# Performance work log

Measured on AMD Instinct MI355X. Metric: run time of the kernel, lower is better.

Reference implementation:

```python
import jax, jax.numpy as jnp
import numpy as np

B, T, H, V = 32, 256, 1024, 256


def setup_inputs() -> dict:
    key = jax.random.key(0)
    ks = jax.random.split(key, 12)
    xavier = float(np.sqrt(6.0 / (H + V)))
    inp = {
        "x": jax.random.randint(ks[0], (B, T), 0, V, dtype=jnp.int64),
        "targets": jax.random.randint(ks[1], (B, T), 0, V, dtype=jnp.int64),
        "h0": jnp.zeros((B, H), jnp.float32),
        "c0": jnp.zeros((B, H), jnp.float32),
        "h1": jnp.zeros((B, H), jnp.float32),
        "c1": jnp.zeros((B, H), jnp.float32),
        # learned params
        "emb": jax.random.normal(ks[2], (V, H), jnp.float32) * 0.05,
        "W_ih0": jax.random.normal(ks[3], (H, 4 * H), jnp.float32) / np.sqrt(H),
        "W_hh0": jax.random.normal(ks[4], (H, 4 * H), jnp.float32) / np.sqrt(H),
        "b0": jnp.zeros((4 * H,), jnp.float32),
        "W_ih1": jax.random.normal(ks[5], (H, 4 * H), jnp.float32) / np.sqrt(H),
        "W_hh1": jax.random.normal(ks[6], (H, 4 * H), jnp.float32) / np.sqrt(H),
        "b1": jnp.zeros((4 * H,), jnp.float32),
        "W_out": jax.random.uniform(ks[7], (H, V), jnp.float32, -xavier, xavier),
        "b_out": jnp.zeros((V,), jnp.float32),
    }
    return inp


def _lstm_cell(h, c, inp, W_ih, W_hh, b):
    # gates: [B, 4H] -> i, f, g, o
    z = inp @ W_ih + h @ W_hh + b
    i, f, g, o = jnp.split(z, 4, axis=-1)
    c_new = jax.nn.sigmoid(f) * c + jax.nn.sigmoid(i) * jnp.tanh(g)
    h_new = jax.nn.sigmoid(o) * jnp.tanh(c_new)
    return h_new, c_new


def reference(x, targets, h0, c0, h1, c1, emb, W_ih0, W_hh0, b0,
              W_ih1, W_hh1, b1, W_out, b_out):
    # Teacher-forcing branch: embed targets, feed embedding at every step.
    embeddings = emb[targets]            # [B, T, H]
    e_seq = jnp.swapaxes(embeddings, 0, 1)  # [T, B, H] for scan over time

    def step(carry, e_t):
        (h0, c0), (h1, c1) = carry
        h0, c0 = _lstm_cell(h0, c0, e_t, W_ih0, W_hh0, b0)
        h1, c1 = _lstm_cell(h1, c1, h0, W_ih1, W_hh1, b1)
        logit = h1 @ W_out + b_out       # [B, V]
        return ((h0, c0), (h1, c1)), logit

    carry0 = ((h0, c0), (h1, c1))
    carry_f, logits_tbv = jax.lax.scan(step, carry0, e_seq)
    logits = jnp.swapaxes(logits_tbv, 0, 1)  # [B, T, V]
    (h0f, c0f), (h1f, c1f) = carry_f
    return logits, h0f, c0f, h1f, c1f
```

## Files before the change

kernel.cpp:

```cpp
#include <hip/hip_runtime.h>
#include <cstdint>


typedef float    f32x4 __attribute__((ext_vector_type(4)));
typedef short    s16x8 __attribute__((ext_vector_type(8)));
typedef unsigned u32x4 __attribute__((ext_vector_type(4)));

#define DEV __device__ __forceinline__

DEV unsigned short f2bf(float x){
  unsigned u = __builtin_bit_cast(unsigned, x);
  unsigned r = (u + 0x7fffu + ((u >> 16) & 1u)) >> 16;
  return (unsigned short)r;
}
DEV float bf2f(unsigned short b){ return __builtin_bit_cast(float, ((unsigned)b) << 16); }

DEV s16x8 ld16(const void* p){ return *(const s16x8*)p; }

DEV f32x4 MF(s16x8 a, s16x8 b, f32x4 c){
  return __builtin_amdgcn_mfma_f32_16x16x32_bf16(a, b, c, 0, 0, 0);
}

#define LDC(dst, ptr)  asm volatile("global_load_dwordx4 %0, %1, off sc0 sc1" : "=v"(dst) : "v"(ptr))
#define LDP(dst, ptr)  asm volatile("global_load_dwordx4 %0, %1, off"         : "=v"(dst) : "v"(ptr))
#define WAITVM(n) do { asm volatile("s_waitcnt vmcnt(" #n ")" ::: "memory"); \
                       __builtin_amdgcn_sched_barrier(0); } while (0)
#define CFENCE()  asm volatile("" ::: "memory")
#define TRIPLE(Cmn, Ahm, Alm, Bhn, Bln) do { \
    Cmn = MF(Ahm, Bhn, Cmn); Cmn = MF(Ahm, Bln, Cmn); Cmn = MF(Alm, Bhn, Cmn); } while (0)

DEV void st16c(void* p, u32x4 v){
  asm volatile("global_store_dwordx4 %0, %1, off sc0 sc1" :: "v"(p), "v"(v) : "memory");
}
DEV void set_flag(int* p, int v){
  __hip_atomic_store(p, v, __ATOMIC_RELAXED, __HIP_MEMORY_SCOPE_AGENT);
}
template<int SLP>
DEV void pollT(const int* f, int lane, int target){
  const int* p0 = f + lane * 8;
  const int* p1 = f + (64 + lane) * 8;
  for (;;) {
    int a = __hip_atomic_load(p0, __ATOMIC_RELAXED, __HIP_MEMORY_SCOPE_AGENT);
    int b = __hip_atomic_load(p1, __ATOMIC_RELAXED, __HIP_MEMORY_SCOPE_AGENT);
    if (__all((a >= target) && (b >= target))) break;
    __builtin_amdgcn_s_sleep(SLP);
  }
  CFENCE();
}
DEV char* h0slot(char* wa0, char* s0, char* hi, int s){
  return (s == 0) ? s0 : ((s <= 128) ? wa0 + ((size_t)(s - 1) << 17)
                                     : hi  + ((size_t)(s - 129) << 17));
}

DEV void halfgemm8(const char* smemMat, const char* ALb, const char* Bb,
                   int wgl, int ksb, int lane, f32x4 (&C)[2][2]) {
  s16x8 P[3][4], AL[3][2];
  #pragma unroll
  for (int d = 0; d < 2; ++d) {
    #pragma unroll
    for (int q = 0; q < 4; ++q) LDP(P[d][q], Bb + ((q * 32 + ksb + d) << 10) + lane * 16);
    LDP(AL[d][0], ALb + ((((wgl * 2 + 0) * 2 + 1) * 32 + ksb + d) << 10) + lane * 16);
    LDP(AL[d][1], ALb + ((((wgl * 2 + 1) * 2 + 1) * 32 + ksb + d) << 10) + lane * 16);
  }
  #pragma unroll
  for (int i = 0; i < 8; ++i) {
    const int ks = ksb + i;
    if (i < 6) {
      #pragma unroll
      for (int q = 0; q < 4; ++q) LDP(P[(i + 2) % 3][q], Bb + ((q * 32 + ks + 2) << 10) + lane * 16);
      LDP(AL[(i + 2) % 3][0], ALb + ((((wgl * 2 + 0) * 2 + 1) * 32 + ks + 2) << 10) + lane * 16);
      LDP(AL[(i + 2) % 3][1], ALb + ((((wgl * 2 + 1) * 2 + 1) * 32 + ks + 2) << 10) + lane * 16);
    }
    s16x8 Ah0 = ld16(smemMat + ((0 * 32 + ks) << 10) + lane * 16);
    s16x8 Ah1 = ld16(smemMat + ((1 * 32 + ks) << 10) + lane * 16);
    if (i < 6) { WAITVM(12); } else if (i == 6) { WAITVM(6); } else { WAITVM(0); }
    TRIPLE(C[0][0], Ah0, AL[i % 3][0], P[i % 3][0], P[i % 3][2]);
    TRIPLE(C[0][1], Ah0, AL[i % 3][0], P[i % 3][1], P[i % 3][3]);
    TRIPLE(C[1][0], Ah1, AL[i % 3][1], P[i % 3][0], P[i % 3][2]);
    TRIPLE(C[1][1], Ah1, AL[i % 3][1], P[i % 3][1], P[i % 3][3]);
  }
}

__global__ void prep_wfrag(const float* __restrict__ W0, const float* __restrict__ W1,
                           const float* __restrict__ W2, const float* __restrict__ W3,
                           char* D0, char* D1, char* D2, char* D3) {
  int gid = blockIdx.x * 256 + threadIdx.x;
  int lane = gid & 63, ks = (gid >> 6) & 31, jb = (gid >> 11) & 255, mat = gid >> 19;
  const float* S = (mat == 0) ? W0 : (mat == 1) ? W1 : (mat == 2) ? W2 : W3;
  char* D = (mat == 0) ? D0 : (mat == 1) ? D1 : (mat == 2) ? D2 : D3;
  int jp = jb * 16 + (lane & 15), u = jp >> 2, g = jp & 3;
  int kb = ks * 32 + (lane >> 4) * 8;
  s16x8 vh, vl;
  #pragma unroll
  for (int i = 0; i < 8; ++i) {
    float x = S[(kb + i) * 4096 + g * 1024 + u];
    unsigned short h = f2bf(x);
    vh[i] = (short)h;
    vl[i] = (short)f2bf(x - bf2f(h));
  }
  *(s16x8*)(D + (((jb * 2 + 0) * 32 + ks) << 10) + lane * 16) = vh;
  *(s16x8*)(D + (((jb * 2 + 1) * 32 + ks) << 10) + lane * 16) = vl;
}

__global__ void prep_bfrag(const float* __restrict__ emb, const float* __restrict__ Wout,
                           char* Demb, char* Dwout) {
  int gid = blockIdx.x * 256 + threadIdx.x;
  int lane = gid & 63, ks = (gid >> 6) & 31, vb = (gid >> 11) & 15, which = gid >> 15;
  int v = vb * 16 + (lane & 15), kb = ks * 32 + (lane >> 4) * 8;
  s16x8 vh, vl;
  #pragma unroll
  for (int i = 0; i < 8; ++i) {
    float x = which ? Wout[(kb + i) * 256 + v] : emb[v * 1024 + kb + i];
    unsigned short h = f2bf(x);
    vh[i] = (short)h;
    vl[i] = (short)f2bf(x - bf2f(h));
  }
  char* D = which ? Dwout : Demb;
  *(s16x8*)(D + (((vb * 2 + 0) * 32 + ks) << 10) + lane * 16) = vh;
  *(s16x8*)(D + (((vb * 2 + 1) * 32 + ks) << 10) + lane * 16) = vl;
}

__global__ void prep_hinit(const float* __restrict__ h0, const float* __restrict__ h1,
                           char* h0s0, char* h1f) {
  int gid = blockIdx.x * 256 + threadIdx.x;
  int lane = gid & 63, ks = (gid >> 6) & 31, nt = (gid >> 11) & 1, which = gid >> 12;
  const float* S = which ? h1 : h0;
  char* D = which ? h1f : h0s0;
  int b = nt * 16 + (lane & 15), kb = ks * 32 + (lane >> 4) * 8;
  s16x8 vh, vl;
  #pragma unroll
  for (int i = 0; i < 8; ++i) {
    float x = S[b * 1024 + kb + i];
    unsigned short h = f2bf(x);
    vh[i] = (short)h;
    vl[i] = (short)f2bf(x - bf2f(h));
  }
  *(s16x8*)(D + (((0 * 2 + nt) * 32 + ks) << 10) + lane * 16) = vh;
  *(s16x8*)(D + (((1 * 2 + nt) * 32 + ks) << 10) + lane * 16) = vl;
}

__global__ void prep_misc(const float* __restrict__ b1, float* b1i, int* f0a, int* f1a) {
  int i = blockIdx.x * 256 + threadIdx.x;
  if (i < 4096) b1i[i] = b1[(i & 3) * 1024 + (i >> 2)];
  if (i < 1024) { f0a[i] = -1; f1a[i] = -1; }
}

__global__ __launch_bounds__(256, 1) void lstm_persist(
    const int* __restrict__ tgt,
    const float* __restrict__ c0_in, const float* __restrict__ c1_in,
    const float* __restrict__ b0, const float* __restrict__ b_out,
    char* __restrict__ WA0, const char* __restrict__ WA1, const char* __restrict__ WA2,
    const char* __restrict__ WAi0, const char* __restrict__ WoutB, const char* __restrict__ embB,
    float* __restrict__ E0, const float* __restrict__ b1i,
    char* __restrict__ h0s0, char* __restrict__ h0hi, char* __restrict__ h1frag,
    int* __restrict__ f0, int* __restrict__ f1,
    float* __restrict__ out)
{
  extern __shared__ char smem[];
  constexpr int PART = 131072;
  constexpr int RP   = 131072 + 16384;
  const int tid = threadIdx.x, lane = tid & 63, wv = tid >> 6;
  const int wg = blockIdx.x;
  const bool isL0 = (wg < 128);
  const int wgl = isL0 ? wg : (wg - 128);
  const int l15 = lane & 15, l4 = lane >> 4;
  const int mi_e = wv >> 1, nt_e = wv & 1;

  __builtin_amdgcn_fence(__ATOMIC_ACQUIRE, "agent");

  if (isL0) {
    u32x4 tmp[8];
    for (int blk = 0; blk < 4; ++blk) {
      #pragma unroll
      for (int q = 0; q < 8; ++q) {
        int idx = tid + (blk * 8 + q) * 256;
        int l16 = idx & 63, ks = (idx >> 6) & 31, mi = (idx >> 11) & 1, part = idx >> 12;
        LDC(tmp[q], WA0 + ((((wgl * 2 + mi) * 2 + part) * 32 + ks) << 10) + l16 * 16);
      }
      WAITVM(0);
      #pragma unroll
      for (int q = 0; q < 8; ++q) {
        int idx = tid + (blk * 8 + q) * 256;
        int l16 = idx & 63, ks = (idx >> 6) & 31, mi = (idx >> 11) & 1, part = idx >> 12;
        *(u32x4*)(smem + (((part * 2 + mi) * 32 + ks) << 10) + l16 * 16) = tmp[q];
      }
    }
  } else {
    for (int idx = tid; idx < 8192; idx += 256) {
      int l16 = idx & 63, ks = (idx >> 6) & 31, mi = (idx >> 11) & 1, mat = idx >> 12;
      const char* W = mat ? WA2 : WA1;
      u32x4 v = *(const u32x4*)(W + ((((wgl * 2 + mi) * 2 + 0) * 32 + ks) << 10) + l16 * 16);
      *(u32x4*)(smem + (((mat * 2 + mi) * 32 + ks) << 10) + l16 * 16) = v;
    }
  }

  if (isL0) {
    f32x4 C[2][4];
    #pragma unroll
    for (int a = 0; a < 2; ++a)
      #pragma unroll
      for (int b = 0; b < 4; ++b) C[a][b] = 0.0f;
    for (int ks = 0; ks < 32; ++ks) {
      s16x8 Ah0, Ah1, Al0, Al1;
      LDC(Ah0, WAi0 + ((((wgl * 2 + 0) * 2 + 0) * 32 + ks) << 10) + lane * 16);
      LDC(Ah1, WAi0 + ((((wgl * 2 + 1) * 2 + 0) * 32 + ks) << 10) + lane * 16);
      LDC(Al0, WAi0 + ((((wgl * 2 + 0) * 2 + 1) * 32 + ks) << 10) + lane * 16);
      LDC(Al1, WAi0 + ((((wgl * 2 + 1) * 2 + 1) * 32 + ks) << 10) + lane * 16);
      WAITVM(0);
      #pragma unroll
      for (int v4 = 0; v4 < 4; ++v4) {
        int vb = wv * 4 + v4;
        s16x8 Bh = ld16(embB + (((vb * 2 + 0) * 32 + ks) << 10) + lane * 16);
        s16x8 Bl = ld16(embB + (((vb * 2 + 1) * 32 + ks) << 10) + lane * 16);
        TRIPLE(C[0][v4], Ah0, Al0, Bh, Bl);
        TRIPLE(C[1][v4], Ah1, Al1, Bh, Bl);
      }
    }
    #pragma unroll
    for (int mi = 0; mi < 2; ++mi) {
      int jb4 = wgl * 32 + mi * 16 + l4 * 4;
      int u = jb4 >> 2;
      f32x4 bb;
      #pragma unroll
      for (int r = 0; r < 4; ++r) bb[r] = b0[r * 1024 + u];
      #pragma unroll
      for (int v4 = 0; v4 < 4; ++v4) {
        int v = (wv * 4 + v4) * 16 + l15;
        *(f32x4*)(E0 + v * 4096 + jb4) = C[mi][v4] + bb;
      }
    }
  }

  float cst;
  {
    const float* cs = isL0 ? c0_in : c1_in;
    cst = cs[(nt_e * 16 + l15) * 1024 + wgl * 8 + mi_e * 4 + l4];
  }
  f32x4 b1z = {0.f, 0.f, 0.f, 0.f};
  if (!isL0) b1z = *(const f32x4*)(b1i + wgl * 32 + mi_e * 16 + (l4 << 2));

  __syncthreads();
  if (tid == 0) set_flag((isL0 ? f0 : f1) + wgl * 8, 0);

  if (isL0) {
    for (int t = 0; t < 256; ++t) {
      const int s = t + 1;
      f32x4 C[2][2];
      #pragma unroll
      for (int a = 0; a < 2; ++a)
        #pragma unroll
        for (int b = 0; b < 2; ++b) C[a][b] = 0.0f;

      int tv = tgt[(nt_e * 16 + l15) * 256 + t];
      f32x4 e0v = *(const f32x4*)(E0 + (size_t)tv * 4096 + wgl * 32 + mi_e * 16 + (l4 << 2));
      pollT<1>(f0, lane, t);
      const char* Bb = h0slot(WA0, h0s0, h0hi, t);
      const int ksb = wv * 8;
      s16x8 P[3][4];
      #pragma unroll
      for (int d = 0; d < 2; ++d)
        #pragma unroll
        for (int q = 0; q < 4; ++q) LDP(P[d][q], Bb + ((q * 32 + ksb + d) << 10) + lane * 16);
      #pragma unroll
      for (int i = 0; i < 8; ++i) {
        const int ks = ksb + i;
        if (i < 6) {
          #pragma unroll
          for (int q = 0; q < 4; ++q) LDP(P[(i + 2) % 3][q], Bb + ((q * 32 + ks + 2) << 10) + lane * 16);
        }
        s16x8 Ah0 = ld16(smem + ((0 * 32 + ks) << 10) + lane * 16);
        s16x8 Ah1 = ld16(smem + ((1 * 32 + ks) << 10) + lane * 16);
        s16x8 Al0 = ld16(smem + ((2 * 32 + ks) << 10) + lane * 16);
        s16x8 Al1 = ld16(smem + ((3 * 32 + ks) << 10) + lane * 16);
        if (i < 6) { WAITVM(8); } else if (i == 6) { WAITVM(4); } else { WAITVM(0); }
        TRIPLE(C[0][0], Ah0, Al0, P[i % 3][0], P[i % 3][2]);
        TRIPLE(C[0][1], Ah0, Al0, P[i % 3][1], P[i % 3][3]);
        TRIPLE(C[1][0], Ah1, Al1, P[i % 3][0], P[i % 3][2]);
        TRIPLE(C[1][1], Ah1, Al1, P[i % 3][1], P[i % 3][3]);
      }

      #pragma unroll
      for (int mi = 0; mi < 2; ++mi)
        #pragma unroll
        for (int nt = 0; nt < 2; ++nt)
          *(f32x4*)(smem + PART + ((wv * 4 + mi * 2 + nt) << 10) + lane * 16) = C[mi][nt];
      __syncthreads();

      {
        f32x4 z = *(const f32x4*)(smem + PART + ((0 * 4 + wv) << 10) + lane * 16);
        #pragma unroll
        for (int w = 1; w < 4; ++w)
          z += *(const f32x4*)(smem + PART + ((w * 4 + wv) << 10) + lane * 16);
        z += e0v;
        float ig = 1.f / (1.f + __expf(-z[0]));
        float fg = 1.f / (1.f + __expf(-z[1]));
        float og = 1.f / (1.f + __expf(-z[3]));
        float cn = fg * cst + ig * tanhf(z[2]);
        float hn = og * tanhf(cn);
        cst = cn;
        unsigned short hb = f2bf(hn);
        unsigned short lb = f2bf(hn - bf2f(hb));
        *(short*)(smem + RP + ((0 + nt_e) * 16 + l15) * 16 + (mi_e * 4 + l4) * 2) = (short)hb;
        *(short*)(smem + RP + ((2 + nt_e) * 16 + l15) * 16 + (mi_e * 4 + l4) * 2) = (short)lb;
        if (t == 255) {
          int u = wgl * 8 + mi_e * 4 + l4, b = nt_e * 16 + l15;
          out[2097152 + b * 1024 + u] = hn;
          out[2097152 + 32768 + b * 1024 + u] = cn;
        }
      }
      __syncthreads();

      if (wv == 0) {
        char* hd = h0slot(WA0, h0s0, h0hi, s);
        u32x4 v = *(const u32x4*)(smem + RP + lane * 16);
        char* dst = hd + (((lane >> 4) * 32 + (wgl >> 2)) << 10) + ((wgl & 3) * 16 + l15) * 16;
        st16c(dst, v);
        asm volatile("s_waitcnt vmcnt(0)" ::: "memory");
        if (lane == 0) set_flag(f0 + wgl * 8, s);
      }
    }
  } else {
    f32x4 zpre;
    {
      pollT<2>(f0, lane, 1);
      f32x4 C2[2][2];
      #pragma unroll
      for (int a = 0; a < 2; ++a)
        #pragma unroll
        for (int b = 0; b < 2; ++b) C2[a][b] = 0.0f;
      halfgemm8(smem, WA1, h0slot(WA0, h0s0, h0hi, 1), wgl, wv * 8, lane, C2);
      #pragma unroll
      for (int mi = 0; mi < 2; ++mi)
        #pragma unroll
        for (int nt = 0; nt < 2; ++nt)
          *(f32x4*)(smem + PART + ((wv * 4 + mi * 2 + nt) << 10) + lane * 16) = C2[mi][nt];
      __syncthreads();
      zpre = *(const f32x4*)(smem + PART + ((0 * 4 + wv) << 10) + lane * 16);
      #pragma unroll
      for (int w = 1; w < 4; ++w)
        zpre += *(const f32x4*)(smem + PART + ((w * 4 + wv) << 10) + lane * 16);
      __syncthreads();
    }

    for (int t = 0; t < 256; ++t) {
      const int s = t + 1;
      f32x4 C[2][2];
      #pragma unroll
      for (int a = 0; a < 2; ++a)
        #pragma unroll
        for (int b = 0; b < 2; ++b) C[a][b] = 0.0f;

      pollT<1>(f1, lane, t);
      halfgemm8(smem + 65536, WA2, h1frag + (size_t)t * 131072, wgl, wv * 8, lane, C);

      #pragma unroll
      for (int mi = 0; mi < 2; ++mi)
        #pragma unroll
        for (int nt = 0; nt < 2; ++nt)
          *(f32x4*)(smem + PART + ((wv * 4 + mi * 2 + nt) << 10) + lane * 16) = C[mi][nt];
      __syncthreads();

      {
        f32x4 z = *(const f32x4*)(smem + PART + ((0 * 4 + wv) << 10) + lane * 16);
        #pragma unroll
        for (int w = 1; w < 4; ++w)
          z += *(const f32x4*)(smem + PART + ((w * 4 + wv) << 10) + lane * 16);
        z += zpre + b1z;
        float ig = 1.f / (1.f + __expf(-z[0]));
        float fg = 1.f / (1.f + __expf(-z[1]));
        float og = 1.f / (1.f + __expf(-z[3]));
        float cn = fg * cst + ig * tanhf(z[2]);
        float hn = og * tanhf(cn);
        cst = cn;
        unsigned short hb = f2bf(hn);
        unsigned short lb = f2bf(hn - bf2f(hb));
        *(short*)(smem + RP + ((0 + nt_e) * 16 + l15) * 16 + (mi_e * 4 + l4) * 2) = (short)hb;
        *(short*)(smem + RP + ((2 + nt_e) * 16 + l15) * 16 + (mi_e * 4 + l4) * 2) = (short)lb;
        if (t == 255) {
          int u = wgl * 8 + mi_e * 4 + l4, b = nt_e * 16 + l15;
          out[2097152 + 65536 + b * 1024 + u] = hn;
          out[2097152 + 65536 + 32768 + b * 1024 + u] = cn;
        }
      }
      __syncthreads();

      if (wv == 0) {
        char* hd = h1frag + (size_t)s * 131072;
        u32x4 v = *(const u32x4*)(smem + RP + lane * 16);
        char* dst = hd + (((lane >> 4) * 32 + (wgl >> 2)) << 10) + ((wgl & 3) * 16 + l15) * 16;
        st16c(dst, v);
        asm volatile("s_waitcnt vmcnt(0)" ::: "memory");
        if (lane == 0) set_flag(f1 + wgl * 8, s);
      }

      if (t < 255) {
        pollT<2>(f0, lane, t + 2);
        f32x4 C2[2][2];
        #pragma unroll
        for (int a = 0; a < 2; ++a)
          #pragma unroll
          for (int b = 0; b < 2; ++b) C2[a][b] = 0.0f;
        halfgemm8(smem, WA1, h0slot(WA0, h0s0, h0hi, t + 2), wgl, wv * 8, lane, C2);
        #pragma unroll
        for (int mi = 0; mi < 2; ++mi)
          #pragma unroll
          for (int nt = 0; nt < 2; ++nt)
            *(f32x4*)(smem + PART + ((wv * 4 + mi * 2 + nt) << 10) + lane * 16) = C2[mi][nt];
        __syncthreads();
        zpre = *(const f32x4*)(smem + PART + ((0 * 4 + wv) << 10) + lane * 16);
        #pragma unroll
        for (int w = 1; w < 4; ++w)
          zpre += *(const f32x4*)(smem + PART + ((w * 4 + wv) << 10) + lane * 16);
        __syncthreads();
      }
    }
  }

  {
    const int tp = isL0 ? wgl : (128 + wgl);
    pollT<32>(f1, lane, tp + 1);
    const char* A = h1frag + (size_t)(tp + 1) * 131072;
    f32x4 C[2][4];
    #pragma unroll
    for (int a = 0; a < 2; ++a)
      #pragma unroll
      for (int b = 0; b < 4; ++b) C[a][b] = 0.0f;
    s16x8 QA[4], QB[4];
    #pragma unroll
    for (int q = 0; q < 4; ++q) LDP(QA[q], A + ((q * 32 + 0) << 10) + lane * 16);
    for (int kk = 0; kk < 16; ++kk) {
      const int ks = kk * 2;
      #pragma unroll
      for (int q = 0; q < 4; ++q) LDP(QB[q], A + ((q * 32 + ks + 1) << 10) + lane * 16);
      asm volatile("s_waitcnt vmcnt(4)" ::: "memory");
      __builtin_amdgcn_sched_barrier(0);
      #pragma unroll
      for (int v4 = 0; v4 < 4; ++v4) {
        int vb = wv * 4 + v4;
        s16x8 Bh = ld16(WoutB + (((vb * 2 + 0) * 32 + ks) << 10) + lane * 16);
        s16x8 Bl = ld16(WoutB + (((vb * 2 + 1) * 32 + ks) << 10) + lane * 16);
        C[0][v4] = MF(QA[0], Bh, C[0][v4]); C[0][v4] = MF(QA[0], Bl, C[0][v4]); C[0][v4] = MF(QA[2], Bh, C[0][v4]);
        C[1][v4] = MF(QA[1], Bh, C[1][v4]); C[1][v4] = MF(QA[1], Bl, C[1][v4]); C[1][v4] = MF(QA[3], Bh, C[1][v4]);
      }
      if (kk < 15) {
        #pragma unroll
        for (int q = 0; q < 4; ++q) LDP(QA[q], A + ((q * 32 + ks + 2) << 10) + lane * 16);
        asm volatile("s_waitcnt vmcnt(4)" ::: "memory");
      } else {
        asm volatile("s_waitcnt vmcnt(0)" ::: "memory");
      }
      __builtin_amdgcn_sched_barrier(0);
      #pragma unroll
      for (int v4 = 0; v4 < 4; ++v4) {
        int vb = wv * 4 + v4;
        s16x8 Bh = ld16(WoutB + (((vb * 2 + 0) * 32 + ks + 1) << 10) + lane * 16);
        s16x8 Bl = ld16(WoutB + (((vb * 2 + 1) * 32 + ks + 1) << 10) + lane * 16);
        C[0][v4] = MF(QB[0], Bh, C[0][v4]); C[0][v4] = MF(QB[0], Bl, C[0][v4]); C[0][v4] = MF(QB[2], Bh, C[0][v4]);
        C[1][v4] = MF(QB[1], Bh, C[1][v4]); C[1][v4] = MF(QB[1], Bl, C[1][v4]); C[1][v4] = MF(QB[3], Bh, C[1][v4]);
      }
    }
    #pragma unroll
    for (int nt = 0; nt < 2; ++nt)
      #pragma unroll
      for (int v4 = 0; v4 < 4; ++v4) {
        int v = (wv * 4 + v4) * 16 + l15;
        float bo = b_out[v];
        #pragma unroll
        for (int r = 0; r < 4; ++r) {
          int b = nt * 16 + l4 * 4 + r;
          out[((size_t)b * 256 + tp) * 256 + v] = C[nt][v4][r] + bo;
        }
      }
  }
}

extern "C" void kernel_launch(void* const* d_in, const int* in_sizes, int n_in,
                              void* d_out, int out_size, void* d_ws, size_t ws_size,
                              hipStream_t stream) {
  const int*   targets = (const int*)d_in[1];
  const float* h0_in   = (const float*)d_in[2];
  const float* c0_in   = (const float*)d_in[3];
  const float* h1_in   = (const float*)d_in[4];
  const float* c1_in   = (const float*)d_in[5];
  const float* emb     = (const float*)d_in[6];
  const float* W_ih0   = (const float*)d_in[7];
  const float* W_hh0   = (const float*)d_in[8];
  const float* b0      = (const float*)d_in[9];
  const float* W_ih1   = (const float*)d_in[10];
  const float* W_hh1   = (const float*)d_in[11];
  const float* b1      = (const float*)d_in[12];
  const float* W_out   = (const float*)d_in[13];
  const float* b_out   = (const float*)d_in[14];
  float* out = (float*)d_out;

  char* ws = (char*)d_ws;
  char*  WA0    = ws;
  char*  WA1    = ws + 16777216;
  char*  WA2    = ws + 33554432;
  char*  WoutB  = ws + 50331648;
  char*  embB   = ws + 51380224;
  float* E0     = (float*)(ws + 52428800);
  float* b1i    = (float*)(ws + 56623104);
  int*   f0     = (int*)(ws + 56639488);
  int*   f1     = (int*)(ws + 56643584);
  char*  h0s0   = ws + 56647680;
  char*  h0hi   = ws + 56778752;
  char*  h1frag = ws + 73555968;
  char*  WAi0   = h1frag + 16777216;

  prep_misc <<<18,   256, 0, stream>>>(b1, b1i, f0, f1);
  prep_wfrag<<<8192, 256, 0, stream>>>(W_hh0, W_ih1, W_hh1, W_ih0, WA0, WA1, WA2, WAi0);
  prep_bfrag<<<256,  256, 0, stream>>>(emb, W_out, embB, WoutB);
  prep_hinit<<<32,   256, 0, stream>>>(h0_in, h1_in, h0s0, h1frag);

  hipFuncSetAttribute(reinterpret_cast<const void*>(lstm_persist),
                      hipFuncAttributeMaxDynamicSharedMemorySize, 148480);
  lstm_persist<<<256, 256, 148480, stream>>>(
      targets, c0_in, c1_in, b0, b_out,
      WA0, WA1, WA2, WAi0, WoutB, embB,
      E0, b1i, h0s0, h0hi, h1frag, f0, f1, out);
}
```

Measured before the change: 1.729 ms.

## Fuse layer-1 recurrent and next-step input GEMMs into one pipelined loop

The layer-1 workgroups used to run two separate half-GEMMs per step: first the recurrent W_hh1·h1, then W_ih1·h0 for step t+2, each with its own poll and barrier pair. They now wait on both flags with one combined poll and interleave both GEMMs in a single software-pipelined load/MFMA loop. The precomputed input contribution is double-buffered in shared memory so it can be summed during the gate computation. W_ih1's high part is no longer cached in LDS and is streamed from global memory instead, which adds global traffic and register pressure and could extend the serial critical path.

```diff
diff --git a/kernel.cpp b/kernel.cpp
--- a/kernel.cpp
+++ b/kernel.cpp
@@ -28,6 +28,11 @@
 #define CFENCE()  asm volatile("" ::: "memory")
 #define TRIPLE(Cmn, Ahm, Alm, Bhn, Bln) do { \
     Cmn = MF(Ahm, Bhn, Cmn); Cmn = MF(Ahm, Bln, Cmn); Cmn = MF(Alm, Bhn, Cmn); } while (0)
+
+template<int N> DEV void waitvm(){
+  __builtin_amdgcn_s_waitcnt((N & 15) | (7 << 4) | (15 << 8) | ((N >> 4) << 14));
+  __builtin_amdgcn_sched_barrier(0);
+}
 
 DEV void st16c(void* p, u32x4 v){
   asm volatile("global_store_dwordx4 %0, %1, off sc0 sc1" :: "v"(p), "v"(v) : "memory");
@@ -47,20 +52,37 @@
   }
   CFENCE();
 }
+DEV void poll2c(const int* fa, int ta, const int* fb, int tb, int lane){
+  const int* a0 = fa + lane * 8;
+  const int* a1 = fa + (64 + lane) * 8;
+  const int* b0 = fb + lane * 8;
+  const int* b1 = fb + (64 + lane) * 8;
+  for (;;) {
+    int x0 = __hip_atomic_load(a0, __ATOMIC_RELAXED, __HIP_MEMORY_SCOPE_AGENT);
+    int x1 = __hip_atomic_load(a1, __ATOMIC_RELAXED, __HIP_MEMORY_SCOPE_AGENT);
+    int y0 = __hip_atomic_load(b0, __ATOMIC_RELAXED, __HIP_MEMORY_SCOPE_AGENT);
+    int y1 = __hip_atomic_load(b1, __ATOMIC_RELAXED, __HIP_MEMORY_SCOPE_AGENT);
+    if (__all((x0 >= ta) && (x1 >= ta) && (y0 >= tb) && (y1 >= tb))) break;
+    __builtin_amdgcn_s_sleep(1);
+  }
+  CFENCE();
+}
 DEV char* h0slot(char* wa0, char* s0, char* hi, int s){
   return (s == 0) ? s0 : ((s <= 128) ? wa0 + ((size_t)(s - 1) << 17)
                                      : hi  + ((size_t)(s - 129) << 17));
 }
 
-DEV void halfgemm8(const char* smemMat, const char* ALb, const char* Bb,
-                   int wgl, int ksb, int lane, f32x4 (&C)[2][2]) {
-  s16x8 P[3][4], AL[3][2];
+DEV void gemm8g(const char* Ab, const char* Bb,
+                int wgl, int ksb, int lane, f32x4 (&C)[2][2]) {
+  s16x8 P[3][4], AH[3][2], AL[3][2];
   #pragma unroll
   for (int d = 0; d < 2; ++d) {
     #pragma unroll
     for (int q = 0; q < 4; ++q) LDP(P[d][q], Bb + ((q * 32 + ksb + d) << 10) + lane * 16);
-    LDP(AL[d][0], ALb + ((((wgl * 2 + 0) * 2 + 1) * 32 + ksb + d) << 10) + lane * 16);
-    LDP(AL[d][1], ALb + ((((wgl * 2 + 1) * 2 + 1) * 32 + ksb + d) << 10) + lane * 16);
+    LDP(AH[d][0], Ab + ((((wgl * 2 + 0) * 2 + 0) * 32 + ksb + d) << 10) + lane * 16);
+    LDP(AH[d][1], Ab + ((((wgl * 2 + 1) * 2 + 0) * 32 + ksb + d) << 10) + lane * 16);
+    LDP(AL[d][0], Ab + ((((wgl * 2 + 0) * 2 + 1) * 32 + ksb + d) << 10) + lane * 16);
+    LDP(AL[d][1], Ab + ((((wgl * 2 + 1) * 2 + 1) * 32 + ksb + d) << 10) + lane * 16);
   }
   #pragma unroll
   for (int i = 0; i < 8; ++i) {
@@ -68,16 +90,16 @@
     if (i < 6) {
       #pragma unroll
       for (int q = 0; q < 4; ++q) LDP(P[(i + 2) % 3][q], Bb + ((q * 32 + ks + 2) << 10) + lane * 16);
-      LDP(AL[(i + 2) % 3][0], ALb + ((((wgl * 2 + 0) * 2 + 1) * 32 + ks + 2) << 10) + lane * 16);
-      LDP(AL[(i + 2) % 3][1], ALb + ((((wgl * 2 + 1) * 2 + 1) * 32 + ks + 2) << 10) + lane * 16);
-    }
-    s16x8 Ah0 = ld16(smemMat + ((0 * 32 + ks) << 10) + lane * 16);
-    s16x8 Ah1 = ld16(smemMat + ((1 * 32 + ks) << 10) + lane * 16);
-    if (i < 6) { WAITVM(12); } else if (i == 6) { WAITVM(6); } else { WAITVM(0); }
-    TRIPLE(C[0][0], Ah0, AL[i % 3][0], P[i % 3][0], P[i % 3][2]);
-    TRIPLE(C[0][1], Ah0, AL[i % 3][0], P[i % 3][1], P[i % 3][3]);
-    TRIPLE(C[1][0], Ah1, AL[i % 3][1], P[i % 3][0], P[i % 3][2]);
-    TRIPLE(C[1][1], Ah1, AL[i % 3][1], P[i % 3][1], P[i % 3][3]);
+      LDP(AH[(i + 2) % 3][0], Ab + ((((wgl * 2 + 0) * 2 + 0) * 32 + ks + 2) << 10) + lane * 16);
+      LDP(AH[(i + 2) % 3][1], Ab + ((((wgl * 2 + 1) * 2 + 0) * 32 + ks + 2) << 10) + lane * 16);
+      LDP(AL[(i + 2) % 3][0], Ab + ((((wgl * 2 + 0) * 2 + 1) * 32 + ks + 2) << 10) + lane * 16);
+      LDP(AL[(i + 2) % 3][1], Ab + ((((wgl * 2 + 1) * 2 + 1) * 32 + ks + 2) << 10) + lane * 16);
+    }
+    if (i < 6) { WAITVM(16); } else if (i == 6) { WAITVM(8); } else { WAITVM(0); }
+    TRIPLE(C[0][0], AH[i % 3][0], AL[i % 3][0], P[i % 3][0], P[i % 3][2]);
+    TRIPLE(C[0][1], AH[i % 3][0], AL[i % 3][0], P[i % 3][1], P[i % 3][3]);
+    TRIPLE(C[1][0], AH[i % 3][1], AL[i % 3][1], P[i % 3][0], P[i % 3][2]);
+    TRIPLE(C[1][1], AH[i % 3][1], AL[i % 3][1], P[i % 3][1], P[i % 3][3]);
   }
 }
 
@@ -157,8 +179,12 @@
     float* __restrict__ out)
 {
   extern __shared__ char smem[];
-  constexpr int PART = 131072;
-  constexpr int RP   = 131072 + 16384;
+  constexpr int PART  = 131072;
+  constexpr int RP0   = 131072 + 16384;
+  constexpr int PART1 = 65536;
+  constexpr int ZTMP  = 81920;
+  constexpr int ZC    = 98304;
+  constexpr int RP1   = 106496;
   const int tid = threadIdx.x, lane = tid & 63, wv = tid >> 6;
   const int wg = blockIdx.x;
   const bool isL0 = (wg < 128);
@@ -186,11 +212,10 @@
       }
     }
   } else {
-    for (int idx = tid; idx < 8192; idx += 256) {
-      int l16 = idx & 63, ks = (idx >> 6) & 31, mi = (idx >> 11) & 1, mat = idx >> 12;
-      const char* W = mat ? WA2 : WA1;
-      u32x4 v = *(const u32x4*)(W + ((((wgl * 2 + mi) * 2 + 0) * 32 + ks) << 10) + l16 * 16);
-      *(u32x4*)(smem + (((mat * 2 + mi) * 32 + ks) << 10) + l16 * 16) = v;
+    for (int idx = tid; idx < 4096; idx += 256) {
+      int l16 = idx & 63, ks = (idx >> 6) & 31, mi = idx >> 11;
+      u32x4 v = *(const u32x4*)(WA2 + ((((wgl * 2 + mi) * 2 + 0) * 32 + ks) << 10) + l16 * 16);
+      *(u32x4*)(smem + ((mi * 32 + ks) << 10) + l16 * 16) = v;
     }
   }
 
@@ -300,8 +325,8 @@
         cst = cn;
         unsigned short hb = f2bf(hn);
         unsigned short lb = f2bf(hn - bf2f(hb));
-        *(short*)(smem + RP + ((0 + nt_e) * 16 + l15) * 16 + (mi_e * 4 + l4) * 2) = (short)hb;
-        *(short*)(smem + RP + ((2 + nt_e) * 16 + l15) * 16 + (mi_e * 4 + l4) * 2) = (short)lb;
+        *(short*)(smem + RP0 + ((0 + nt_e) * 16 + l15) * 16 + (mi_e * 4 + l4) * 2) = (short)hb;
+        *(short*)(smem + RP0 + ((2 + nt_e) * 16 + l15) * 16 + (mi_e * 4 + l4) * 2) = (short)lb;
         if (t == 255) {
           int u = wgl * 8 + mi_e * 4 + l4, b = nt_e * 16 + l15;
           out[2097152 + b * 1024 + u] = hn;
@@ -312,7 +337,7 @@
 
       if (wv == 0) {
         char* hd = h0slot(WA0, h0s0, h0hi, s);
-        u32x4 v = *(const u32x4*)(smem + RP + lane * 16);
+        u32x4 v = *(const u32x4*)(smem + RP0 + lane * 16);
         char* dst = hd + (((lane >> 4) * 32 + (wgl >> 2)) << 10) + ((wgl & 3) * 16 + l15) * 16;
         st16c(dst, v);
         asm volatile("s_waitcnt vmcnt(0)" ::: "memory");
@@ -320,7 +345,6 @@
       }
     }
   } else {
-    f32x4 zpre;
     {
       pollT<2>(f0, lane, 1);
       f32x4 C2[2][2];
@@ -328,44 +352,88 @@
       for (int a = 0; a < 2; ++a)
         #pragma unroll
         for (int b = 0; b < 2; ++b) C2[a][b] = 0.0f;
-      halfgemm8(smem, WA1, h0slot(WA0, h0s0, h0hi, 1), wgl, wv * 8, lane, C2);
+      gemm8g(WA1, h0slot(WA0, h0s0, h0hi, 1), wgl, wv * 8, lane, C2);
       #pragma unroll
       for (int mi = 0; mi < 2; ++mi)
         #pragma unroll
         for (int nt = 0; nt < 2; ++nt)
-          *(f32x4*)(smem + PART + ((wv * 4 + mi * 2 + nt) << 10) + lane * 16) = C2[mi][nt];
+          *(f32x4*)(smem + ZTMP + ((wv * 4 + mi * 2 + nt) << 10) + lane * 16) = C2[mi][nt];
       __syncthreads();
-      zpre = *(const f32x4*)(smem + PART + ((0 * 4 + wv) << 10) + lane * 16);
-      #pragma unroll
-      for (int w = 1; w < 4; ++w)
-        zpre += *(const f32x4*)(smem + PART + ((w * 4 + wv) << 10) + lane * 16);
+      f32x4 zq = {0.f, 0.f, 0.f, 0.f};
+      #pragma unroll
+      for (int w = 0; w < 4; ++w)
+        zq += *(const f32x4*)(smem + ZTMP + ((w * 4 + wv) << 10) + lane * 16);
+      *(f32x4*)(smem + ZC + ((0 * 4 + wv) << 10) + lane * 16) = zq;
       __syncthreads();
     }
 
     for (int t = 0; t < 256; ++t) {
       const int s = t + 1;
-      f32x4 C[2][2];
+      const int cur = t & 1, nxt = cur ^ 1;
+      const int tz = (t < 255) ? (t + 2) : 256;
+      f32x4 C[2][2], C2[2][2];
       #pragma unroll
       for (int a = 0; a < 2; ++a)
         #pragma unroll
-        for (int b = 0; b < 2; ++b) C[a][b] = 0.0f;
-
-      pollT<1>(f1, lane, t);
-      halfgemm8(smem + 65536, WA2, h1frag + (size_t)t * 131072, wgl, wv * 8, lane, C);
+        for (int b = 0; b < 2; ++b) { C[a][b] = 0.0f; C2[a][b] = 0.0f; }
+
+      poll2c(f1, t, f0, tz, lane);
+
+      const char* B1 = h1frag + (size_t)t * 131072;
+      const char* B2 = h0slot(WA0, h0s0, h0hi, tz);
+      const int ksb = wv * 8;
+      s16x8 P1[3][4], AL1[3][2], AH2[3][2], AL2[3][2], P2[3][4];
+#define ISS(d, dst) { const int kk = ksb + (d); \
+      LDP(P1[dst][0], B1 + ((0 * 32 + kk) << 10) + lane * 16); \
+      LDP(P1[dst][1], B1 + ((1 * 32 + kk) << 10) + lane * 16); \
+      LDP(P1[dst][2], B1 + ((2 * 32 + kk) << 10) + lane * 16); \
+      LDP(P1[dst][3], B1 + ((3 * 32 + kk) << 10) + lane * 16); \
+      LDP(AL1[dst][0], WA2 + ((((wgl * 2 + 0) * 2 + 1) * 32 + kk) << 10) + lane * 16); \
+      LDP(AL1[dst][1], WA2 + ((((wgl * 2 + 1) * 2 + 1) * 32 + kk) << 10) + lane * 16); \
+      LDP(AH2[dst][0], WA1 + ((((wgl * 2 + 0) * 2 + 0) * 32 + kk) << 10) + lane * 16); \
+      LDP(AH2[dst][1], WA1 + ((((wgl * 2 + 1) * 2 + 0) * 32 + kk) << 10) + lane * 16); \
+      LDP(AL2[dst][0], WA1 + ((((wgl * 2 + 0) * 2 + 1) * 32 + kk) << 10) + lane * 16); \
+      LDP(AL2[dst][1], WA1 + ((((wgl * 2 + 1) * 2 + 1) * 32 + kk) << 10) + lane * 16); \
+      LDP(P2[dst][0], B2 + ((0 * 32 + kk) << 10) + lane * 16); \
+      LDP(P2[dst][1], B2 + ((1 * 32 + kk) << 10) + lane * 16); \
+      LDP(P2[dst][2], B2 + ((2 * 32 + kk) << 10) + lane * 16); \
+      LDP(P2[dst][3], B2 + ((3 * 32 + kk) << 10) + lane * 16); }
+      ISS(0, 0)
+      ISS(1, 1)
+      #pragma unroll
+      for (int i = 0; i < 8; ++i) {
+        const int ks = ksb + i;
+        if (i < 6) ISS(i + 2, (i + 2) % 3)
+        s16x8 Ah0c = ld16(smem + ((0 * 32 + ks) << 10) + lane * 16);
+        s16x8 Ah1c = ld16(smem + ((1 * 32 + ks) << 10) + lane * 16);
+        if (i < 6) { waitvm<28>(); } else if (i == 6) { waitvm<14>(); } else { waitvm<0>(); }
+        TRIPLE(C[0][0], Ah0c, AL1[i % 3][0], P1[i % 3][0], P1[i % 3][2]);
+        TRIPLE(C[0][1], Ah0c, AL1[i % 3][0], P1[i % 3][1], P1[i % 3][3]);
+        TRIPLE(C[1][0], Ah1c, AL1[i % 3][1], P1[i % 3][0], P1[i % 3][2]);
+        TRIPLE(C[1][1], Ah1c, AL1[i % 3][1], P1[i % 3][1], P1[i % 3][3]);
+        TRIPLE(C2[0][0], AH2[i % 3][0], AL2[i % 3][0], P2[i % 3][0], P2[i % 3][2]);
+        TRIPLE(C2[0][1], AH2[i % 3][0], AL2[i % 3][0], P2[i % 3][1], P2[i % 3][3]);
+        TRIPLE(C2[1][0], AH2[i % 3][1], AL2[i % 3][1], P2[i % 3][0], P2[i % 3][2]);
+        TRIPLE(C2[1][1], AH2[i % 3][1], AL2[i % 3][1], P2[i % 3][1], P2[i % 3][3]);
+      }
+#undef ISS
 
       #pragma unroll
       for (int mi = 0; mi < 2; ++mi)
         #pragma unroll
-        for (int nt = 0; nt < 2; ++nt)
-          *(f32x4*)(smem + PART + ((wv * 4 + mi * 2 + nt) << 10) + lane * 16) = C[mi][nt];
+        for (int nt = 0; nt < 2; ++nt) {
+          *(f32x4*)(smem + PART1 + ((wv * 4 + mi * 2 + nt) << 10) + lane * 16) = C[mi][nt];
+          *(f32x4*)(smem + ZTMP  + ((wv * 4 + mi * 2 + nt) << 10) + lane * 16) = C2[mi][nt];
+        }
       __syncthreads();
 
       {
-        f32x4 z = *(const f32x4*)(smem + PART + ((0 * 4 + wv) << 10) + lane * 16);
-        #pragma unroll
-        for (int w = 1; w < 4; ++w)
-          z += *(const f32x4*)(smem + PART + ((w * 4 + wv) << 10) + lane * 16);
-        z += zpre + b1z;
+        f32x4 z = {0.f, 0.f, 0.f, 0.f};
+        #pragma unroll
+        for (int w = 0; w < 4; ++w)
+          z += *(const f32x4*)(smem + PART1 + ((w * 4 + wv) << 10) + lane * 16);
+        z += *(const f32x4*)(smem + ZC + ((cur * 4 + wv) << 10) + lane * 16);
+        z += b1z;
         float ig = 1.f / (1.f + __expf(-z[0]));
         float fg = 1.f / (1.f + __expf(-z[1]));
         float og = 1.f / (1.f + __expf(-z[3]));
@@ -374,44 +442,28 @@
         cst = cn;
         unsigned short hb = f2bf(hn);
         unsigned short lb = f2bf(hn - bf2f(hb));
-        *(short*)(smem + RP + ((0 + nt_e) * 16 + l15) * 16 + (mi_e * 4 + l4) * 2) = (short)hb;
-        *(short*)(smem + RP + ((2 + nt_e) * 16 + l15) * 16 + (mi_e * 4 + l4) * 2) = (short)lb;
+        *(short*)(smem + RP1 + ((0 + nt_e) * 16 + l15) * 16 + (mi_e * 4 + l4) * 2) = (short)hb;
+        *(short*)(smem + RP1 + ((2 + nt_e) * 16 + l15) * 16 + (mi_e * 4 + l4) * 2) = (short)lb;
         if (t == 255) {
           int u = wgl * 8 + mi_e * 4 + l4, b = nt_e * 16 + l15;
           out[2097152 + 65536 + b * 1024 + u] = hn;
           out[2097152 + 65536 + 32768 + b * 1024 + u] = cn;
         }
+        f32x4 zq = {0.f, 0.f, 0.f, 0.f};
+        #pragma unroll
+        for (int w = 0; w < 4; ++w)
+          zq += *(const f32x4*)(smem + ZTMP + ((w * 4 + wv) << 10) + lane * 16);
+        *(f32x4*)(smem + ZC + ((nxt * 4 + wv) << 10) + lane * 16) = zq;
       }
       __syncthreads();
 
       if (wv == 0) {
         char* hd = h1frag + (size_t)s * 131072;
-        u32x4 v = *(const u32x4*)(smem + RP + lane * 16);
+        u32x4 v = *(const u32x4*)(smem + RP1 + lane * 16);
         char* dst = hd + (((lane >> 4) * 32 + (wgl >> 2)) << 10) + ((wgl & 3) * 16 + l15) * 16;
         st16c(dst, v);
         asm volatile("s_waitcnt vmcnt(0)" ::: "memory");
         if (lane == 0) set_flag(f1 + wgl * 8, s);
-      }
-
-      if (t < 255) {
-        pollT<2>(f0, lane, t + 2);
-        f32x4 C2[2][2];
-        #pragma unroll
-        for (int a = 0; a < 2; ++a)
-          #pragma unroll
-          for (int b = 0; b < 2; ++b) C2[a][b] = 0.0f;
-        halfgemm8(smem, WA1, h0slot(WA0, h0s0, h0hi, t + 2), wgl, wv * 8, lane, C2);
-        #pragma unroll
-        for (int mi = 0; mi < 2; ++mi)
-          #pragma unroll
-          for (int nt = 0; nt < 2; ++nt)
-            *(f32x4*)(smem + PART + ((wv * 4 + mi * 2 + nt) << 10) + lane * 16) = C2[mi][nt];
-        __syncthreads();
-        zpre = *(const f32x4*)(smem + PART + ((0 * 4 + wv) << 10) + lane * 16);
-        #pragma unroll
-        for (int w = 1; w < 4; ++w)
-          zpre += *(const f32x4*)(smem + PART + ((w * 4 + wv) << 10) + lane * 16);
-        __syncthreads();
       }
     }
   }
```

Result: slower. 2.412 ms (+39.5%).
